# Kernel optimization log

Measured on AMD Instinct MI355X. Metric: run time of the kernel, lower is better.

Reference implementation:

```python
import jax, jax.numpy as jnp
import numpy as np

B, N, C, H, W = 2, 512, 32, 200, 200
THRESH = 0.05
# BEVCamera: x_range=y_range=(-1,1) -> FoV=2 meters; sh = H/FoVy = 100, sw = W/FoVx = 100
SH = H / 2.0
SW = W / 2.0
LOWPASS = 0.3        # 3DGS low-pass filter added to 2D cov diagonal
ALPHA_MIN = 1.0 / 255.0
ALPHA_MAX = 0.99


def setup_inputs() -> dict:
    key = jax.random.key(0)
    k1, k2, k3, k4 = jax.random.split(key, 4)
    features = jax.random.normal(k1, (B, N, C), dtype=jnp.float32)
    means3D = jax.random.uniform(k2, (B, N, 3), dtype=jnp.float32, minval=-1.0, maxval=1.0)
    # build PSD 3D covariances: Sigma = A A^T + eps*I, store 6 upper-tri entries
    A = 0.05 * jax.random.normal(k3, (B, N, 3, 3), dtype=jnp.float32)
    S = jnp.einsum('bnij,bnkj->bnik', A, A) + 1e-4 * jnp.eye(3, dtype=jnp.float32)
    cov3D = jnp.stack([S[..., 0, 0], S[..., 0, 1], S[..., 0, 2],
                       S[..., 1, 1], S[..., 1, 2], S[..., 2, 2]], axis=-1)
    opacities = jax.random.uniform(k4, (B, N, 1), dtype=jnp.float32)
    return {"features": features, "means3D": means3D, "cov3D": cov3D, "opacities": opacities}


def _render_one(features, means3D, cov3D, op):
    # features [N,C], means3D [N,3], cov3D [N,6] (xx,xy,xz,yy,yz,zz), op [N,1]
    dtype = features.dtype
    opac = op[:, 0]
    opac = jnp.where(opac > THRESH, opac, 0.0)  # masked-out gaussians contribute nothing
    # projmatrix: u = H/2 - sh*y (height), v = W/2 - sw*x (width)
    mu_u = H / 2.0 - SH * means3D[:, 1]
    mu_v = W / 2.0 - SW * means3D[:, 0]
    # 2D covariance from orthographic BEV projection J = [[0,-sh,0],[-sw,0,0]]
    Cuu = SH * SH * cov3D[:, 3] + LOWPASS
    Cvv = SW * SW * cov3D[:, 0] + LOWPASS
    Cuv = SH * SW * cov3D[:, 1]
    det = Cuu * Cvv - Cuv * Cuv
    valid = det > 0.0
    inv_det = jnp.where(valid, 1.0 / jnp.where(valid, det, 1.0), 0.0)
    Iuu = Cvv * inv_det
    Ivv = Cuu * inv_det
    Iuv = -Cuv * inv_det
    opac = jnp.where(valid, opac, 0.0)
    uu = jnp.arange(H, dtype=dtype)
    vv = jnp.arange(W, dtype=dtype)
    du = uu[None, :, None] - mu_u[:, None, None]   # [N,H,1]
    dv = vv[None, None, :] - mu_v[:, None, None]   # [N,1,W]
    power = (-0.5 * (Iuu[:, None, None] * du * du + Ivv[:, None, None] * dv * dv)
             - Iuv[:, None, None] * du * dv)       # [N,H,W]
    alpha = jnp.minimum(ALPHA_MAX, opac[:, None, None] * jnp.exp(jnp.minimum(power, 0.0)))
    alpha = jnp.where((power > 0.0) | (alpha < ALPHA_MIN), 0.0, alpha)
    # front-to-back alpha compositing in gaussian index order (all depths are 0 -> stable sort)
    logt = jnp.log1p(-alpha)                       # [N,H,W]
    T = jnp.exp(jnp.cumsum(logt, axis=0) - logt)   # exclusive transmittance
    w = T * alpha                                  # [N,H,W]
    return jnp.einsum('nhw,nc->chw', w, features)  # bg color is zeros


def reference(features, means3D, cov3D, opacities):
    bev = jax.vmap(_render_one)(features, means3D, cov3D, opacities)  # [B,C,H,W]
    num_gaussians = (opacities[..., 0] > THRESH).astype(jnp.float32).sum(axis=-1).mean()
    return bev, num_gaussians
```

## Files before the change

### kernel.cpp

```cpp
#include <hip/hip_runtime.h>
#include <math.h>

#define B_ 2
#define N_ 512
#define C_ 32
#define H_ 200
#define W_ 200
#define HW_ (H_*W_)
#define THRESH_ 0.05f
#define OUT_BEV (B_*C_*H_*W_)
#define NSEG 4
#define TILES_PER_B 625
#define LOG2E 1.4426950408889634f
#define LN2   0.6931471805599453f

__device__ __forceinline__ float rlane(float x, int l) {
    return __int_as_float(__builtin_amdgcn_readlane(__float_as_int(x), l));
}

__device__ __forceinline__ bool pcompute(
    const float* __restrict__ m3, const float* __restrict__ cv,
    const float* __restrict__ opc, int i,
    float tu0, float tu1, float tv0, float tv1,
    float& mu_u, float& mu_v, float& a2, float& b2, float& c2,
    float& opo, float& thr2)
{
    float x  = m3[i*3 + 0];
    float y  = m3[i*3 + 1];
    float c0 = cv[i*6 + 0];
    float c1 = cv[i*6 + 1];
    float c3 = cv[i*6 + 3];
    float op = opc[i];
    mu_u = 100.0f - 100.0f * y;
    mu_v = 100.0f - 100.0f * x;
    float Cuu = 10000.0f * c3 + 0.3f;
    float Cvv = 10000.0f * c0 + 0.3f;
    float Cuv = 10000.0f * c1;
    float det = Cuu * Cvv - Cuv * Cuv;
    bool valid = det > 0.0f;
    float opac = (op > THRESH_) ? op : 0.0f;
    if (!valid) opac = 0.0f;
    float inv_det = valid ? (1.0f / det) : 0.0f;
    a2 = -0.5f * LOG2E * (Cvv * inv_det);
    b2 = -0.5f * LOG2E * (Cuu * inv_det);
    c2 =  LOG2E * (Cuv * inv_det);
    opo = opac;
    if (opac > 0.0f) {
        float r2 = log2f(255.0f * opac);
        thr2 = -r2;
        float rn = LN2 * r2;
        float du_max = sqrtf(fmaxf(2.0f * rn * Cuu, 0.0f)) + 1.0e-3f;
        float dv_max = sqrtf(fmaxf(2.0f * rn * Cvv, 0.0f)) + 1.0e-3f;
        return (mu_u - du_max <= tu1) & (mu_u + du_max >= tu0) &
               (mu_v - dv_max <= tv1) & (mu_v + dv_max >= tv0);
    }
    thr2 = 3.0e38f;
    return false;
}

#define WALK(mask, P, base_n)                                                \
    while (mask) {                                                           \
        int j0 = __builtin_ctzll(mask); mask &= mask - 1;                    \
        bool two = (mask != 0ull);                                           \
        int j1 = two ? __builtin_ctzll(mask) : j0;                           \
        if (two) mask &= mask - 1;                                           \
        float mu_u0 = rlane(P##_mu_u, j0), mu_v0 = rlane(P##_mu_v, j0);      \
        float a0 = rlane(P##_a, j0), b0 = rlane(P##_b, j0);                  \
        float c0 = rlane(P##_c, j0), op0 = rlane(P##_op, j0);                \
        float th0 = rlane(P##_th, j0);                                       \
        float mu_u1 = rlane(P##_mu_u, j1), mu_v1 = rlane(P##_mu_v, j1);      \
        float a1 = rlane(P##_a, j1), b1 = rlane(P##_b, j1);                  \
        float c1 = rlane(P##_c, j1), op1 = rlane(P##_op, j1);                \
        float th1 = rlane(P##_th, j1);                                       \
        const float* f0 = featB + (size_t)((base_n) + j0) * C_;              \
        const float* f1 = featB + (size_t)((base_n) + j1) * C_;              \
        float du0 = u - mu_u0, dv0 = v - mu_v0;                              \
        float pw0 = fmaf(a0 * du0, du0, fmaf(b0 * dv0, dv0, c0 * (du0 * dv0))); \
        bool hit0 = (pw0 <= 0.0f) && (pw0 >= th0);                           \
        float al0 = hit0 ? fminf(0.99f, op0 * exp2f(pw0)) : 0.0f;            \
        float du1 = u - mu_u1, dv1 = v - mu_v1;                              \
        float pw1 = fmaf(a1 * du1, du1, fmaf(b1 * dv1, dv1, c1 * (du1 * dv1))); \
        bool hit1 = two && (pw1 <= 0.0f) && (pw1 >= th1);                    \
        float al1 = hit1 ? fminf(0.99f, op1 * exp2f(pw1)) : 0.0f;            \
        if (__any(hit0 | hit1)) {                                            \
            float w0 = T * al0;                                              \
            float Tm = T * (1.0f - al0);                                     \
            float w1 = Tm * al1;                                             \
            T = Tm * (1.0f - al1);                                           \
            _Pragma("unroll")                                                \
            for (int c = 0; c < C_; ++c)                                     \
                acc[c] = fmaf(w1, f1[c], fmaf(w0, f0[c], acc[c]));           \
        }                                                                    \
    }

__global__ __launch_bounds__(256, 5) void render_kernel(
    const float* __restrict__ features,
    const float* __restrict__ means3D,
    const float* __restrict__ cov3D,
    const float* __restrict__ opacities,
    float* __restrict__ out)
{
    __shared__ float s_T[NSEG][64];
    __shared__ float s_W[NSEG * 64];
    __shared__ float s_acc[NSEG][8][64];

    int blk = blockIdx.x;
    int tid = threadIdx.x;

    if (blk == B_ * TILES_PER_B) {
        int cnt = ((opacities[tid]       > THRESH_) ? 1 : 0)
                + ((opacities[tid + 256] > THRESH_) ? 1 : 0)
                + ((opacities[tid + 512] > THRESH_) ? 1 : 0)
                + ((opacities[tid + 768] > THRESH_) ? 1 : 0);
        for (int off = 32; off > 0; off >>= 1) cnt += __shfl_down(cnt, off);
        int* s_red = (int*)s_W;
        if ((tid & 63) == 0) s_red[tid >> 6] = cnt;
        __syncthreads();
        if (tid == 0)
            out[OUT_BEV] = (float)(s_red[0] + s_red[1] + s_red[2] + s_red[3]) * 0.5f;
        return;
    }

    int b  = blk / TILES_PER_B;
    int t  = blk - b * TILES_PER_B;
    int tu = t / 25;
    int tv = t - tu * 25;
    int wave = __builtin_amdgcn_readfirstlane(tid >> 6);
    int lane = tid & 63;

    float tu0 = (float)(tu * 8), tu1 = tu0 + 7.0f;
    float tv0 = (float)(tv * 8), tv1 = tv0 + 7.0f;

    float A_mu_u, A_mu_v, A_a, A_b, A_c, A_op, A_th;
    float B_mu_u, B_mu_v, B_a, B_b, B_c, B_op, B_th;
    int i0 = b * N_ + wave * 128 + lane;
    bool ovA = pcompute(means3D, cov3D, opacities, i0,      tu0, tu1, tv0, tv1,
                        A_mu_u, A_mu_v, A_a, A_b, A_c, A_op, A_th);
    bool ovB = pcompute(means3D, cov3D, opacities, i0 + 64, tu0, tu1, tv0, tv1,
                        B_mu_u, B_mu_v, B_a, B_b, B_c, B_op, B_th);
    unsigned long long m0 = __ballot(ovA);
    unsigned long long m1 = __ballot(ovB);

    int uu = tu * 8 + (lane >> 3);
    int vv = tv * 8 + (lane & 7);
    float u = (float)uu, v = (float)vv;

    float T = 1.0f;
    float acc[C_];
#pragma unroll
    for (int c = 0; c < C_; ++c) acc[c] = 0.0f;
    const float* featB = features + (size_t)b * (N_ * C_);

    WALK(m0, A, wave * 128)
    WALK(m1, B, wave * 128 + 64)

    s_T[wave][lane] = T;
    __syncthreads();

    {
        float Wg = 1.0f;
        for (int g = 0; g < wave; ++g) Wg *= s_T[g][lane];
        s_W[wave * 64 + lane] = Wg;
    }

    size_t obase = (size_t)b * C_ * HW_ + (size_t)(tu * 8) * W_ + (size_t)(tv * 8);
    size_t opix  = (size_t)(lane >> 3) * W_ + (lane & 7);
#pragma unroll
    for (int k = 0; k < 4; ++k) {
#pragma unroll
        for (int cc = 0; cc < 8; ++cc) s_acc[wave][cc][lane] = acc[k * 8 + cc];
        __syncthreads();
        float v0 = 0.0f, v1 = 0.0f;
#pragma unroll
        for (int g = 0; g < NSEG; ++g) {
            float wgt = s_W[g * 64 + lane];
            v0 = fmaf(wgt, s_acc[g][wave][lane],     v0);
            v1 = fmaf(wgt, s_acc[g][wave + 4][lane], v1);
        }
        out[obase + (size_t)(k * 8 + wave) * HW_ + opix]     = v0;
        out[obase + (size_t)(k * 8 + wave + 4) * HW_ + opix] = v1;
        if (k < 3) __syncthreads();
    }
}

extern "C" void kernel_launch(void* const* d_in, const int* in_sizes, int n_in,
                              void* d_out, int out_size, void* d_ws, size_t ws_size,
                              hipStream_t stream) {
    const float* features  = (const float*)d_in[0];
    const float* means3D   = (const float*)d_in[1];
    const float* cov3D     = (const float*)d_in[2];
    const float* opacities = (const float*)d_in[3];
    float* out = (float*)d_out;
    render_kernel<<<B_ * TILES_PER_B + 1, 256, 0, stream>>>(
        features, means3D, cov3D, opacities, out);
}
```

Before: 16.91 us.

## Compact overlapping gaussians into LDS list and use packed FMA accumulation

Each wave stream-compacts the parameters of tile-overlapping gaussians into shared memory using mbcnt prefix positions. The inner loop then reads parameters from LDS one gaussian per iteration instead of issuing seven readlanes per gaussian. It also drops the per-pair __any skip branch and accumulates the 32 channels as packed 2-wide FMAs. The epilogue reduction reuses the same shared buffer and runs in two rounds instead of four. The price is more LDS traffic and a loop that no longer skips pairs with no hits.

```diff
diff --git a/kernel.cpp b/kernel.cpp
--- a/kernel.cpp
+++ b/kernel.cpp
@@ -14,16 +14,12 @@
 #define LOG2E 1.4426950408889634f
 #define LN2   0.6931471805599453f
 
-__device__ __forceinline__ float rlane(float x, int l) {
-    return __int_as_float(__builtin_amdgcn_readlane(__float_as_int(x), l));
-}
+typedef float v2f __attribute__((ext_vector_type(2)));
 
 __device__ __forceinline__ bool pcompute(
     const float* __restrict__ m3, const float* __restrict__ cv,
     const float* __restrict__ opc, int i,
-    float tu0, float tu1, float tv0, float tv1,
-    float& mu_u, float& mu_v, float& a2, float& b2, float& c2,
-    float& opo, float& thr2)
+    float tu0, float tu1, float tv0, float tv1, float4& q0, float4& q1)
 {
     float x  = m3[i*3 + 0];
     float y  = m3[i*3 + 1];
@@ -31,8 +27,8 @@
     float c1 = cv[i*6 + 1];
     float c3 = cv[i*6 + 3];
     float op = opc[i];
-    mu_u = 100.0f - 100.0f * y;
-    mu_v = 100.0f - 100.0f * x;
+    float mu_u = 100.0f - 100.0f * y;
+    float mu_v = 100.0f - 100.0f * x;
     float Cuu = 10000.0f * c3 + 0.3f;
     float Cvv = 10000.0f * c0 + 0.3f;
     float Cuv = 10000.0f * c1;
@@ -41,57 +37,24 @@
     float opac = (op > THRESH_) ? op : 0.0f;
     if (!valid) opac = 0.0f;
     float inv_det = valid ? (1.0f / det) : 0.0f;
-    a2 = -0.5f * LOG2E * (Cvv * inv_det);
-    b2 = -0.5f * LOG2E * (Cuu * inv_det);
-    c2 =  LOG2E * (Cuv * inv_det);
-    opo = opac;
+    float a2 = -0.5f * LOG2E * (Cvv * inv_det);
+    float b2 = -0.5f * LOG2E * (Cuu * inv_det);
+    float c2 =  LOG2E * (Cuv * inv_det);
+    float thr2 = 3.0e38f;
+    bool ov = false;
     if (opac > 0.0f) {
         float r2 = log2f(255.0f * opac);
         thr2 = -r2;
         float rn = LN2 * r2;
         float du_max = sqrtf(fmaxf(2.0f * rn * Cuu, 0.0f)) + 1.0e-3f;
         float dv_max = sqrtf(fmaxf(2.0f * rn * Cvv, 0.0f)) + 1.0e-3f;
-        return (mu_u - du_max <= tu1) & (mu_u + du_max >= tu0) &
-               (mu_v - dv_max <= tv1) & (mu_v + dv_max >= tv0);
-    }
-    thr2 = 3.0e38f;
-    return false;
+        ov = (mu_u - du_max <= tu1) & (mu_u + du_max >= tu0) &
+             (mu_v - dv_max <= tv1) & (mu_v + dv_max >= tv0);
+    }
+    q0 = make_float4(mu_u, mu_v, a2, b2);
+    q1 = make_float4(c2, opac, thr2, 0.0f);
+    return ov;
 }
-
-#define WALK(mask, P, base_n)                                                \
-    while (mask) {                                                           \
-        int j0 = __builtin_ctzll(mask); mask &= mask - 1;                    \
-        bool two = (mask != 0ull);                                           \
-        int j1 = two ? __builtin_ctzll(mask) : j0;                           \
-        if (two) mask &= mask - 1;                                           \
-        float mu_u0 = rlane(P##_mu_u, j0), mu_v0 = rlane(P##_mu_v, j0);      \
-        float a0 = rlane(P##_a, j0), b0 = rlane(P##_b, j0);                  \
-        float c0 = rlane(P##_c, j0), op0 = rlane(P##_op, j0);                \
-        float th0 = rlane(P##_th, j0);                                       \
-        float mu_u1 = rlane(P##_mu_u, j1), mu_v1 = rlane(P##_mu_v, j1);      \
-        float a1 = rlane(P##_a, j1), b1 = rlane(P##_b, j1);                  \
-        float c1 = rlane(P##_c, j1), op1 = rlane(P##_op, j1);                \
-        float th1 = rlane(P##_th, j1);                                       \
-        const float* f0 = featB + (size_t)((base_n) + j0) * C_;              \
-        const float* f1 = featB + (size_t)((base_n) + j1) * C_;              \
-        float du0 = u - mu_u0, dv0 = v - mu_v0;                              \
-        float pw0 = fmaf(a0 * du0, du0, fmaf(b0 * dv0, dv0, c0 * (du0 * dv0))); \
-        bool hit0 = (pw0 <= 0.0f) && (pw0 >= th0);                           \
-        float al0 = hit0 ? fminf(0.99f, op0 * exp2f(pw0)) : 0.0f;            \
-        float du1 = u - mu_u1, dv1 = v - mu_v1;                              \
-        float pw1 = fmaf(a1 * du1, du1, fmaf(b1 * dv1, dv1, c1 * (du1 * dv1))); \
-        bool hit1 = two && (pw1 <= 0.0f) && (pw1 >= th1);                    \
-        float al1 = hit1 ? fminf(0.99f, op1 * exp2f(pw1)) : 0.0f;            \
-        if (__any(hit0 | hit1)) {                                            \
-            float w0 = T * al0;                                              \
-            float Tm = T * (1.0f - al0);                                     \
-            float w1 = Tm * al1;                                             \
-            T = Tm * (1.0f - al1);                                           \
-            _Pragma("unroll")                                                \
-            for (int c = 0; c < C_; ++c)                                     \
-                acc[c] = fmaf(w1, f1[c], fmaf(w0, f0[c], acc[c]));           \
-        }                                                                    \
-    }
 
 __global__ __launch_bounds__(256, 5) void render_kernel(
     const float* __restrict__ features,
@@ -102,7 +65,9 @@
 {
     __shared__ float s_T[NSEG][64];
     __shared__ float s_W[NSEG * 64];
-    __shared__ float s_acc[NSEG][8][64];
+    __shared__ float4 u_mem[NSEG * 128 * 2];
+    float4* s_hit = u_mem;
+    float (*s_acc)[16][64] = (float (*)[16][64])u_mem;
 
     int blk = blockIdx.x;
     int tid = threadIdx.x;
@@ -131,28 +96,61 @@
     float tu0 = (float)(tu * 8), tu1 = tu0 + 7.0f;
     float tv0 = (float)(tv * 8), tv1 = tv0 + 7.0f;
 
-    float A_mu_u, A_mu_v, A_a, A_b, A_c, A_op, A_th;
-    float B_mu_u, B_mu_v, B_a, B_b, B_c, B_op, B_th;
+    float4 qA0, qA1, qB0, qB1;
     int i0 = b * N_ + wave * 128 + lane;
-    bool ovA = pcompute(means3D, cov3D, opacities, i0,      tu0, tu1, tv0, tv1,
-                        A_mu_u, A_mu_v, A_a, A_b, A_c, A_op, A_th);
-    bool ovB = pcompute(means3D, cov3D, opacities, i0 + 64, tu0, tu1, tv0, tv1,
-                        B_mu_u, B_mu_v, B_a, B_b, B_c, B_op, B_th);
+    bool ovA = pcompute(means3D, cov3D, opacities, i0,      tu0, tu1, tv0, tv1, qA0, qA1);
+    bool ovB = pcompute(means3D, cov3D, opacities, i0 + 64, tu0, tu1, tv0, tv1, qB0, qB1);
     unsigned long long m0 = __ballot(ovA);
     unsigned long long m1 = __ballot(ovB);
+
+    int sbase = wave * 256;
+    {
+        int posA = __builtin_amdgcn_mbcnt_hi((unsigned)(m0 >> 32),
+                   __builtin_amdgcn_mbcnt_lo((unsigned)m0, 0));
+        if (ovA) { int s = sbase + 2 * posA; s_hit[s] = qA0; s_hit[s + 1] = qA1; }
+        int cA = __popcll(m0);
+        int posB = __builtin_amdgcn_mbcnt_hi((unsigned)(m1 >> 32),
+                   __builtin_amdgcn_mbcnt_lo((unsigned)m1, 0));
+        if (ovB) { int s = sbase + 2 * (cA + posB); s_hit[s] = qB0; s_hit[s + 1] = qB1; }
+    }
 
     int uu = tu * 8 + (lane >> 3);
     int vv = tv * 8 + (lane & 7);
     float u = (float)uu, v = (float)vv;
 
     float T = 1.0f;
-    float acc[C_];
-#pragma unroll
-    for (int c = 0; c < C_; ++c) acc[c] = 0.0f;
+    v2f acc2[16];
+#pragma unroll
+    for (int i = 0; i < 16; ++i) acc2[i] = (v2f){0.0f, 0.0f};
+
     const float* featB = features + (size_t)b * (N_ * C_);
-
-    WALK(m0, A, wave * 128)
-    WALK(m1, B, wave * 128 + 64)
+    int nh = __builtin_amdgcn_readfirstlane(__popcll(m0) + __popcll(m1));
+    unsigned long long w0 = m0, w1 = m1;
+    int nbase = wave * 128;
+
+#pragma unroll 2
+    for (int k = 0; k < nh; ++k) {
+        float4 q0 = s_hit[sbase + 2 * k];
+        float4 q1 = s_hit[sbase + 2 * k + 1];
+        bool useA = (w0 != 0ull);
+        unsigned long long m = useA ? w0 : w1;
+        int j = __builtin_ctzll(m);
+        int n = nbase + (useA ? j : 64 + j);
+        if (useA) w0 &= w0 - 1; else w1 &= w1 - 1;
+        n = __builtin_amdgcn_readfirstlane(n);
+        const v2f* f2 = (const v2f*)(featB + (size_t)n * C_);
+        float du = u - q0.x;
+        float dv = v - q0.y;
+        float pw = fmaf(q0.z * du, du, fmaf(q0.w * dv, dv, q1.x * (du * dv)));
+        bool hit = (pw <= 0.0f) && (pw >= q1.z);
+        float al = hit ? fminf(0.99f, q1.y * exp2f(pw)) : 0.0f;
+        float wgt = T * al;
+        v2f w2 = {wgt, wgt};
+#pragma unroll
+        for (int i = 0; i < 16; ++i)
+            acc2[i] = __builtin_elementwise_fma(w2, f2[i], acc2[i]);
+        T *= (1.0f - al);
+    }
 
     s_T[wave][lane] = T;
     __syncthreads();
@@ -166,20 +164,27 @@
     size_t obase = (size_t)b * C_ * HW_ + (size_t)(tu * 8) * W_ + (size_t)(tv * 8);
     size_t opix  = (size_t)(lane >> 3) * W_ + (lane & 7);
 #pragma unroll
-    for (int k = 0; k < 4; ++k) {
-#pragma unroll
-        for (int cc = 0; cc < 8; ++cc) s_acc[wave][cc][lane] = acc[k * 8 + cc];
+    for (int k = 0; k < 2; ++k) {
+#pragma unroll
+        for (int cc = 0; cc < 8; ++cc) {
+            v2f a = acc2[k * 8 + cc];
+            s_acc[wave][cc * 2][lane]     = a.x;
+            s_acc[wave][cc * 2 + 1][lane] = a.y;
+        }
         __syncthreads();
-        float v0 = 0.0f, v1 = 0.0f;
-#pragma unroll
-        for (int g = 0; g < NSEG; ++g) {
-            float wgt = s_W[g * 64 + lane];
-            v0 = fmaf(wgt, s_acc[g][wave][lane],     v0);
-            v1 = fmaf(wgt, s_acc[g][wave + 4][lane], v1);
+        float vq[4];
+#pragma unroll
+        for (int q = 0; q < 4; ++q) {
+            float s = 0.0f;
+#pragma unroll
+            for (int g = 0; g < NSEG; ++g)
+                s = fmaf(s_W[g * 64 + lane], s_acc[g][wave * 4 + q][lane], s);
+            vq[q] = s;
         }
-        out[obase + (size_t)(k * 8 + wave) * HW_ + opix]     = v0;
-        out[obase + (size_t)(k * 8 + wave + 4) * HW_ + opix] = v1;
-        if (k < 3) __syncthreads();
+#pragma unroll
+        for (int q = 0; q < 4; ++q)
+            out[obase + (size_t)(k * 16 + wave * 4 + q) * HW_ + opix] = vq[q];
+        if (k == 0) __syncthreads();
     }
 }
 
```

After: 17.25 us. Within noise of the previous version (+2.0%).

## Pack per-segment accumulators to bf16 in LDS and use packed FMA

Applied to the files above, without the earlier changes.

The per-channel accumulation loop now runs on two-wide float vectors so the compiler can emit packed FMAs. At the end, each wave's 32 channel partials are converted to bf16 pairs and written to shared memory in a single pass, so only one barrier is needed instead of one per channel group. The transmittance prefix is computed directly in registers. Reducing the partial accumulators to bf16 loses precision in the output and may exceed the reference tolerance.

```diff
diff --git a/kernel.cpp b/kernel.cpp
--- a/kernel.cpp
+++ b/kernel.cpp
@@ -13,6 +13,8 @@
 #define TILES_PER_B 625
 #define LOG2E 1.4426950408889634f
 #define LN2   0.6931471805599453f
+
+typedef float v2f __attribute__((ext_vector_type(2)));
 
 __device__ __forceinline__ float rlane(float x, int l) {
     return __int_as_float(__builtin_amdgcn_readlane(__float_as_int(x), l));
@@ -72,8 +74,8 @@
         float a1 = rlane(P##_a, j1), b1 = rlane(P##_b, j1);                  \
         float c1 = rlane(P##_c, j1), op1 = rlane(P##_op, j1);                \
         float th1 = rlane(P##_th, j1);                                       \
-        const float* f0 = featB + (size_t)((base_n) + j0) * C_;              \
-        const float* f1 = featB + (size_t)((base_n) + j1) * C_;              \
+        const v2f* f0 = (const v2f*)(featB + (size_t)((base_n) + j0) * C_);  \
+        const v2f* f1 = (const v2f*)(featB + (size_t)((base_n) + j1) * C_);  \
         float du0 = u - mu_u0, dv0 = v - mu_v0;                              \
         float pw0 = fmaf(a0 * du0, du0, fmaf(b0 * dv0, dv0, c0 * (du0 * dv0))); \
         bool hit0 = (pw0 <= 0.0f) && (pw0 >= th0);                           \
@@ -87,9 +89,11 @@
             float Tm = T * (1.0f - al0);                                     \
             float w1 = Tm * al1;                                             \
             T = Tm * (1.0f - al1);                                           \
+            v2f w0v = {w0, w0}, w1v = {w1, w1};                              \
             _Pragma("unroll")                                                \
-            for (int c = 0; c < C_; ++c)                                     \
-                acc[c] = fmaf(w1, f1[c], fmaf(w0, f0[c], acc[c]));           \
+            for (int i = 0; i < 16; ++i)                                     \
+                acc2[i] = __builtin_elementwise_fma(w1v, f1[i],              \
+                          __builtin_elementwise_fma(w0v, f0[i], acc2[i]));   \
         }                                                                    \
     }
 
@@ -101,8 +105,7 @@
     float* __restrict__ out)
 {
     __shared__ float s_T[NSEG][64];
-    __shared__ float s_W[NSEG * 64];
-    __shared__ float s_acc[NSEG][8][64];
+    __shared__ unsigned int s_pk[NSEG * 16 * 64];
 
     int blk = blockIdx.x;
     int tid = threadIdx.x;
@@ -113,7 +116,7 @@
                 + ((opacities[tid + 512] > THRESH_) ? 1 : 0)
                 + ((opacities[tid + 768] > THRESH_) ? 1 : 0);
         for (int off = 32; off > 0; off >>= 1) cnt += __shfl_down(cnt, off);
-        int* s_red = (int*)s_W;
+        int* s_red = (int*)s_T;
         if ((tid & 63) == 0) s_red[tid >> 6] = cnt;
         __syncthreads();
         if (tid == 0)
@@ -146,40 +149,47 @@
     float u = (float)uu, v = (float)vv;
 
     float T = 1.0f;
-    float acc[C_];
-#pragma unroll
-    for (int c = 0; c < C_; ++c) acc[c] = 0.0f;
+    v2f acc2[16];
+#pragma unroll
+    for (int i = 0; i < 16; ++i) acc2[i] = (v2f){0.0f, 0.0f};
     const float* featB = features + (size_t)b * (N_ * C_);
 
     WALK(m0, A, wave * 128)
     WALK(m1, B, wave * 128 + 64)
 
     s_T[wave][lane] = T;
+#pragma unroll
+    for (int i = 0; i < 16; ++i) {
+        unsigned int r;
+        asm("v_cvt_pk_bf16_f32 %0, %1, %2"
+            : "=v"(r) : "v"(acc2[i].x), "v"(acc2[i].y));
+        s_pk[(wave * 16 + i) * 64 + lane] = r;
+    }
     __syncthreads();
 
-    {
-        float Wg = 1.0f;
-        for (int g = 0; g < wave; ++g) Wg *= s_T[g][lane];
-        s_W[wave * 64 + lane] = Wg;
-    }
+    float t0g = s_T[0][lane], t1g = s_T[1][lane], t2g = s_T[2][lane];
+    float Wg[NSEG];
+    Wg[0] = 1.0f;
+    Wg[1] = t0g;
+    Wg[2] = t0g * t1g;
+    Wg[3] = Wg[2] * t2g;
 
     size_t obase = (size_t)b * C_ * HW_ + (size_t)(tu * 8) * W_ + (size_t)(tv * 8);
     size_t opix  = (size_t)(lane >> 3) * W_ + (lane & 7);
 #pragma unroll
-    for (int k = 0; k < 4; ++k) {
-#pragma unroll
-        for (int cc = 0; cc < 8; ++cc) s_acc[wave][cc][lane] = acc[k * 8 + cc];
-        __syncthreads();
-        float v0 = 0.0f, v1 = 0.0f;
+    for (int q = 0; q < 4; ++q) {
+        int pr = wave * 4 + q;
+        float vlo = 0.0f, vhi = 0.0f;
 #pragma unroll
         for (int g = 0; g < NSEG; ++g) {
-            float wgt = s_W[g * 64 + lane];
-            v0 = fmaf(wgt, s_acc[g][wave][lane],     v0);
-            v1 = fmaf(wgt, s_acc[g][wave + 4][lane], v1);
+            unsigned int r = s_pk[(g * 16 + pr) * 64 + lane];
+            float flo = __uint_as_float(r << 16);
+            float fhi = __uint_as_float(r & 0xffff0000u);
+            vlo = fmaf(Wg[g], flo, vlo);
+            vhi = fmaf(Wg[g], fhi, vhi);
         }
-        out[obase + (size_t)(k * 8 + wave) * HW_ + opix]     = v0;
-        out[obase + (size_t)(k * 8 + wave + 4) * HW_ + opix] = v1;
-        if (k < 3) __syncthreads();
+        out[obase + (size_t)(2 * pr)     * HW_ + opix] = vlo;
+        out[obase + (size_t)(2 * pr + 1) * HW_ + opix] = vhi;
     }
 }
 
```

Measured after the change: 16.84 us. Within noise of the previous version (-0.4%).
